# Kernel tuning notes

Measured on AMD Instinct MI355X. Metric: run time of the kernel, lower is better.

## Reference

```python
import jax, jax.numpy as jnp
import numpy as np

D_MODEL = 1024
NUM_HEADS = 16
D_K = D_MODEL // NUM_HEADS
B, S = 4, 2048


def setup_inputs() -> dict:
    key = jax.random.key(0)
    ks = jax.random.split(key, 11)
    scale = 1.0 / np.sqrt(D_MODEL)
    inp = {
        'query': jax.random.normal(ks[0], (B, S, D_MODEL), dtype=jnp.float32),
        'key':   jax.random.normal(ks[1], (B, S, D_MODEL), dtype=jnp.float32),
        'value': jax.random.normal(ks[2], (B, S, D_MODEL), dtype=jnp.float32),
        'Wq': jax.random.normal(ks[3], (D_MODEL, D_MODEL), dtype=jnp.float32) * scale,
        'bq': jnp.zeros((D_MODEL,), dtype=jnp.float32),
        'Wk': jax.random.normal(ks[4], (D_MODEL, D_MODEL), dtype=jnp.float32) * scale,
        'bk': jnp.zeros((D_MODEL,), dtype=jnp.float32),
        'Wv': jax.random.normal(ks[5], (D_MODEL, D_MODEL), dtype=jnp.float32) * scale,
        'bv': jnp.zeros((D_MODEL,), dtype=jnp.float32),
        'Wo': jax.random.normal(ks[6], (D_MODEL, D_MODEL), dtype=jnp.float32) * scale,
        'bo': jnp.zeros((D_MODEL,), dtype=jnp.float32),
    }
    return inp


def reference(query, key, value, Wq, bq, Wk, bk, Wv, bv, Wo, bo):
    b, sq, _ = query.shape
    sk = key.shape[1]
    # projections (torch Linear: x @ W.T + b; here W stored as [in, out])
    Q = query @ Wq + bq
    K = key @ Wk + bk
    V = value @ Wv + bv
    # split heads: [b, h, s, d_k]
    Q = Q.reshape(b, sq, NUM_HEADS, D_K).transpose(0, 2, 1, 3)
    K = K.reshape(b, sk, NUM_HEADS, D_K).transpose(0, 2, 1, 3)
    V = V.reshape(b, sk, NUM_HEADS, D_K).transpose(0, 2, 1, 3)
    # scaled dot-product attention (full [b,h,sq,sk] scores, as in source)
    scores = jnp.einsum('bhqd,bhkd->bhqk', Q, K) / jnp.sqrt(jnp.float32(D_K))
    attn = jax.nn.softmax(scores, axis=-1)
    out = jnp.einsum('bhqk,bhkd->bhqd', attn, V)
    out = out.transpose(0, 2, 1, 3).reshape(b, sq, D_MODEL)
    return out @ Wo + bo
```

## Files before the change

### kernel.cpp

```cpp
#include <hip/hip_runtime.h>
#include <hip/hip_bf16.h>
#include <stdint.h>

typedef __bf16 bf16x8 __attribute__((ext_vector_type(8)));
typedef __bf16 bf16x4 __attribute__((ext_vector_type(4)));
typedef float  f32x4  __attribute__((ext_vector_type(4)));
typedef unsigned short u16;

#define D_MODEL 1024
#define NUM_HEADS 16
#define DK 64
#define BATCH 4
#define SEQ 2048
#define M_TOTAL (BATCH*SEQ)
#define QK_SCALE 0.18033688011112042f

static __device__ __forceinline__ u16 f2bf(float f) {
    __bf16 h = (__bf16)f;
    return __builtin_bit_cast(u16, h);
}

#define ASYNC16(gptr, lptr) __builtin_amdgcn_global_load_lds( \
    (const __attribute__((address_space(1))) unsigned*)(uintptr_t)(gptr), \
    (__attribute__((address_space(3))) unsigned*)(unsigned)(uintptr_t)(lptr), 16, 0, 0)

__global__ void detect_dtype(const u16* __restrict__ q, unsigned* __restrict__ flag) {
    __shared__ int sh[256];
    int cnt = 0;
    for (int i = threadIdx.x; i < 8192; i += 256) {
        u16 v = q[2 * i];
        int e = (v >> 7) & 0xFF;
        if (e >= 100 && e <= 134) cnt++;
    }
    sh[threadIdx.x] = cnt;
    __syncthreads();
    for (int s = 128; s > 0; s >>= 1) {
        if (threadIdx.x < s) sh[threadIdx.x] += sh[threadIdx.x + s];
        __syncthreads();
    }
    if (threadIdx.x == 0) *flag = (sh[0] > 4096) ? 1u : 0u;
}

__global__ void transpose_w(const u16* __restrict__ W0, const u16* __restrict__ W1,
                            const u16* __restrict__ W2, const u16* __restrict__ W3,
                            u16* __restrict__ WT, const unsigned* __restrict__ flagp) {
    __shared__ u16 tile[32][33];
    const u16* W = (blockIdx.z == 0) ? W0 : (blockIdx.z == 1) ? W1 : (blockIdx.z == 2) ? W2 : W3;
    u16* T = WT + (size_t)blockIdx.z * D_MODEL * D_MODEL;
    bool is_bf16 = (*flagp != 0);
    int x = threadIdx.x, y0 = threadIdx.y;
    int bx = blockIdx.x * 32, by = blockIdx.y * 32;
    if (is_bf16) {
#pragma unroll
        for (int i = 0; i < 4; i++) {
            int y = y0 + i * 8;
            tile[y][x] = W[(size_t)(by + y) * D_MODEL + bx + x];
        }
    } else {
        const float* Wf = (const float*)W;
#pragma unroll
        for (int i = 0; i < 4; i++) {
            int y = y0 + i * 8;
            tile[y][x] = f2bf(Wf[(size_t)(by + y) * D_MODEL + bx + x]);
        }
    }
    __syncthreads();
#pragma unroll
    for (int i = 0; i < 4; i++) {
        int y = y0 + i * 8;
        T[(size_t)(bx + y) * D_MODEL + by + x] = tile[x][y];
    }
}

__global__ __launch_bounds__(256) void gemm_qkv(
    const u16* __restrict__ qin, const u16* __restrict__ kin, const u16* __restrict__ vin,
    const u16* __restrict__ WT,
    const u16* __restrict__ bq, const u16* __restrict__ bk, const u16* __restrict__ bv,
    u16* __restrict__ Qp, u16* __restrict__ Kp, u16* __restrict__ VpT,
    const unsigned* __restrict__ flagp)
{
    __shared__ __align__(16) u16 As[128 * 32];
    __shared__ __align__(16) u16 Bs[128 * 32];
    const int id  = blockIdx.x;
    const int xcd = id & 7, j = id >> 3;
    const int zy  = xcd * 24 + (j >> 3);
    const int bx  = j & 7;
    const int z   = zy >> 6, by = zy & 63;

    const u16* A    = (z == 0) ? qin : (z == 1) ? kin : vin;
    const u16* W    = WT + (size_t)z * 1048576;
    const u16* bias = (z == 0) ? bq : (z == 1) ? bk : bv;
    u16* C          = (z == 0) ? Qp : (z == 1) ? Kp : VpT;
    const int transV = (z == 2);
    const float oscale = (z == 0) ? QK_SCALE : 1.0f;

    const int tid  = threadIdx.x;
    const int lane = tid & 63, w = tid >> 6;
    const int quad = lane >> 4, l15 = lane & 15;
    const int wm = w >> 1, wn = w & 1;
    const int m_blk = by * 128, n_blk = bx * 128;
    const bool is_bf16 = (*flagp != 0);

    f32x4 acc[4][4] = {};

    const int ch0 = w * 2, ch1 = w * 2 + 1;
    const int sr0 = ch0 * 16 + (lane >> 2), sr1 = ch1 * 16 + (lane >> 2);
    const int skp = (lane & 3) * 8;
    const int frow = tid >> 1, fkp = (tid & 1) * 16;
    const float* Af = (const float*)A;

    for (int k0 = 0; k0 < D_MODEL; k0 += 32) {
        if (!is_bf16) {
            const float* src = Af + (size_t)(m_blk + frow) * D_MODEL + k0 + fkp;
            float4 f0 = ((const float4*)src)[0];
            float4 f1 = ((const float4*)src)[1];
            float4 f2 = ((const float4*)src)[2];
            float4 f3 = ((const float4*)src)[3];
            bf16x8 p0, p1;
            p0[0] = (__bf16)f0.x; p0[1] = (__bf16)f0.y; p0[2] = (__bf16)f0.z; p0[3] = (__bf16)f0.w;
            p0[4] = (__bf16)f1.x; p0[5] = (__bf16)f1.y; p0[6] = (__bf16)f1.z; p0[7] = (__bf16)f1.w;
            p1[0] = (__bf16)f2.x; p1[1] = (__bf16)f2.y; p1[2] = (__bf16)f2.z; p1[3] = (__bf16)f2.w;
            p1[4] = (__bf16)f3.x; p1[5] = (__bf16)f3.y; p1[6] = (__bf16)f3.z; p1[7] = (__bf16)f3.w;
            *(bf16x8*)&As[frow * 32 + fkp]     = p0;
            *(bf16x8*)&As[frow * 32 + fkp + 8] = p1;
        } else {
            ASYNC16(A + (size_t)(m_blk + sr0) * D_MODEL + k0 + skp, &As[ch0 * 512]);
            ASYNC16(A + (size_t)(m_blk + sr1) * D_MODEL + k0 + skp, &As[ch1 * 512]);
        }
        ASYNC16(W + (size_t)(n_blk + sr0) * D_MODEL + k0 + skp, &Bs[ch0 * 512]);
        ASYNC16(W + (size_t)(n_blk + sr1) * D_MODEL + k0 + skp, &Bs[ch1 * 512]);
        __syncthreads();

        bf16x8 af[4], bg[4];
#pragma unroll
        for (int sm = 0; sm < 4; sm++)
            af[sm] = *(const bf16x8*)&As[(wm * 64 + sm * 16 + l15) * 32 + quad * 8];
#pragma unroll
        for (int sn = 0; sn < 4; sn++)
            bg[sn] = *(const bf16x8*)&Bs[(wn * 64 + sn * 16 + l15) * 32 + quad * 8];
#pragma unroll
        for (int sm = 0; sm < 4; sm++)
#pragma unroll
            for (int sn = 0; sn < 4; sn++)
                acc[sm][sn] = __builtin_amdgcn_mfma_f32_16x16x32_bf16(af[sm], bg[sn], acc[sm][sn], 0, 0, 0);
        __syncthreads();
    }

#pragma unroll
    for (int sn = 0; sn < 4; sn++) {
        int n = n_blk + wn * 64 + sn * 16 + l15;
        float bvf = is_bf16 ? (float)((const __bf16*)bias)[n] : ((const float*)bias)[n];
#pragma unroll
        for (int sm = 0; sm < 4; sm++) {
            int mrow = m_blk + wm * 64 + sm * 16 + quad * 4;
            if (transV) {
                int b = mrow >> 11, s = mrow & 2047;
                ushort4 pk;
                pk.x = f2bf(acc[sm][sn][0] + bvf);
                pk.y = f2bf(acc[sm][sn][1] + bvf);
                pk.z = f2bf(acc[sm][sn][2] + bvf);
                pk.w = f2bf(acc[sm][sn][3] + bvf);
                *(ushort4*)(C + (size_t)b * D_MODEL * SEQ + (size_t)n * SEQ + s) = pk;
            } else {
#pragma unroll
                for (int r = 0; r < 4; r++)
                    C[(size_t)(mrow + r) * D_MODEL + n] = f2bf((acc[sm][sn][r] + bvf) * oscale);
            }
        }
    }
}

__global__ __launch_bounds__(256) void gemm_o(
    const u16* __restrict__ A, const u16* __restrict__ WT,
    const u16* __restrict__ bias, u16* __restrict__ C,
    const unsigned* __restrict__ flagp)
{
    __shared__ __align__(16) u16 As[64 * 32];
    __shared__ __align__(16) u16 Bs[128 * 32];
    const int id  = blockIdx.x;
    const int xcd = id & 7, j = id >> 3;
    const int by  = xcd * 16 + (j >> 3);
    const int bx  = j & 7;

    const int tid  = threadIdx.x;
    const int lane = tid & 63, w = tid >> 6;
    const int quad = lane >> 4, l15 = lane & 15;
    const int wm = w >> 1, wn = w & 1;
    const int m_blk = by * 64, n_blk = bx * 128;
    const bool is_bf16 = (*flagp != 0);

    f32x4 acc[2][4] = {};
    const int srow = lane >> 2, skp = (lane & 3) * 8;

    for (int k0 = 0; k0 < D_MODEL; k0 += 32) {
#pragma unroll
        for (int i = 0; i < 3; i++) {
            int c = w * 3 + i;
            if (c < 4)
                ASYNC16(A  + (size_t)(m_blk + c * 16 + srow) * D_MODEL + k0 + skp, &As[c * 512]);
            else
                ASYNC16(WT + (size_t)(n_blk + (c - 4) * 16 + srow) * D_MODEL + k0 + skp, &Bs[(c - 4) * 512]);
        }
        __syncthreads();

        bf16x8 af[2], bg[4];
#pragma unroll
        for (int sm = 0; sm < 2; sm++)
            af[sm] = *(const bf16x8*)&As[(wm * 32 + sm * 16 + l15) * 32 + quad * 8];
#pragma unroll
        for (int sn = 0; sn < 4; sn++)
            bg[sn] = *(const bf16x8*)&Bs[(wn * 64 + sn * 16 + l15) * 32 + quad * 8];
#pragma unroll
        for (int sm = 0; sm < 2; sm++)
#pragma unroll
            for (int sn = 0; sn < 4; sn++)
                acc[sm][sn] = __builtin_amdgcn_mfma_f32_16x16x32_bf16(af[sm], bg[sn], acc[sm][sn], 0, 0, 0);
        __syncthreads();
    }

#pragma unroll
    for (int sn = 0; sn < 4; sn++) {
        int n = n_blk + wn * 64 + sn * 16 + l15;
        float bvf = is_bf16 ? (float)((const __bf16*)bias)[n] : ((const float*)bias)[n];
#pragma unroll
        for (int sm = 0; sm < 2; sm++) {
            int mrow = m_blk + wm * 32 + sm * 16 + quad * 4;
            if (!is_bf16) {
                float* Cf = (float*)C;
#pragma unroll
                for (int r = 0; r < 4; r++)
                    Cf[(size_t)(mrow + r) * D_MODEL + n] = acc[sm][sn][r] + bvf;
            } else {
#pragma unroll
                for (int r = 0; r < 4; r++)
                    C[(size_t)(mrow + r) * D_MODEL + n] = f2bf(acc[sm][sn][r] + bvf);
            }
        }
    }
}

__global__ __launch_bounds__(256) void attn_kernel(
    const u16* __restrict__ Qp, const u16* __restrict__ Kp,
    const u16* __restrict__ VpT, u16* __restrict__ AO)
{
    __shared__ __align__(16) u16 Ks[2][64 * 64];
    __shared__ __align__(16) u16 Vs[2][64 * 64];
    __shared__ __align__(16) u16 Ps[4][32][68];
    const int id  = blockIdx.x;
    const int xcd = id & 7, j = id >> 3;
    const int bh  = xcd * 8 + (j >> 4);
    const int qx  = j & 15;

    const int tid  = threadIdx.x;
    const int lane = tid & 63, w = tid >> 6;
    const int quad = lane >> 4, l15 = lane & 15;
    const int b = bh >> 4, h = bh & 15;
    const int q_base = qx * 128 + w * 32;

    bf16x8 bQ[2][2];
#pragma unroll
    for (int sn = 0; sn < 2; sn++)
#pragma unroll
        for (int ds = 0; ds < 2; ds++)
            bQ[sn][ds] = *(const bf16x8*)(Qp + (size_t)(b * SEQ + q_base + sn * 16 + l15) * D_MODEL
                                              + h * DK + ds * 32 + quad * 8);

    float lsum[2] = {0.0f, 0.0f};
    f32x4 OT[2][4] = {};

    const u16* Kbase = Kp  + (size_t)(b * SEQ) * D_MODEL + h * DK;
    const u16* Vbase = VpT + (size_t)b * D_MODEL * SEQ + (size_t)(h * DK) * SEQ;

    const int c0   = w * 2;
    const int lrow = lane >> 3;
    const int ug   = (lane & 7) ^ lrow;
    const int swz  = l15 & 7;

    auto issue_tile = [&](int key0, int bf) {
#pragma unroll
        for (int i = 0; i < 2; i++) {
            int c = c0 + i;
            ASYNC16(Kbase + (size_t)(key0 + c * 8 + lrow) * D_MODEL + ug * 8, &Ks[bf][c * 512]);
            ASYNC16(Vbase + (size_t)(c * 8 + lrow) * SEQ + key0 + ug * 8,     &Vs[bf][c * 512]);
        }
    };

    issue_tile(0, 0);
    __syncthreads();

    for (int t = 0; t < SEQ / 64; t++) {
        const int cur = t & 1;
        if (t + 1 < SEQ / 64) issue_tile((t + 1) * 64, cur ^ 1);

#pragma unroll
        for (int kc = 0; kc < 4; kc++) {
            const int krow = (kc * 16 + l15) * 64;
            bf16x8 k0 = *(const bf16x8*)&Ks[cur][krow + ((quad ^ swz) * 8)];
            bf16x8 k1 = *(const bf16x8*)&Ks[cur][krow + (((4 + quad) ^ swz) * 8)];
#pragma unroll
            for (int sn = 0; sn < 2; sn++) {
                f32x4 s = {};
                s = __builtin_amdgcn_mfma_f32_16x16x32_bf16(k0, bQ[sn][0], s, 0, 0, 0);
                s = __builtin_amdgcn_mfma_f32_16x16x32_bf16(k1, bQ[sn][1], s, 0, 0, 0);
                float p0 = __builtin_amdgcn_exp2f(s[0]);
                float p1 = __builtin_amdgcn_exp2f(s[1]);
                float p2 = __builtin_amdgcn_exp2f(s[2]);
                float p3 = __builtin_amdgcn_exp2f(s[3]);
                lsum[sn] += (p0 + p1) + (p2 + p3);
                bf16x4 pk;
                pk[0] = (__bf16)p0; pk[1] = (__bf16)p1; pk[2] = (__bf16)p2; pk[3] = (__bf16)p3;
                *(bf16x4*)&Ps[w][sn * 16 + l15][kc * 16 + quad * 4] = pk;
            }
        }

#pragma unroll
        for (int kc2 = 0; kc2 < 2; kc2++) {
            bf16x8 bP0 = *(const bf16x8*)&Ps[w][l15][kc2 * 32 + quad * 8];
            bf16x8 bP1 = *(const bf16x8*)&Ps[w][16 + l15][kc2 * 32 + quad * 8];
#pragma unroll
            for (int nd = 0; nd < 4; nd++) {
                bf16x8 aV = *(const bf16x8*)&Vs[cur][(nd * 16 + l15) * 64
                                                    + (((kc2 * 4 + quad) ^ swz) * 8)];
                OT[0][nd] = __builtin_amdgcn_mfma_f32_16x16x32_bf16(aV, bP0, OT[0][nd], 0, 0, 0);
                OT[1][nd] = __builtin_amdgcn_mfma_f32_16x16x32_bf16(aV, bP1, OT[1][nd], 0, 0, 0);
            }
        }
        __syncthreads();
    }

#pragma unroll
    for (int sn = 0; sn < 2; sn++) {
        lsum[sn] += __shfl_xor(lsum[sn], 16, 64);
        lsum[sn] += __shfl_xor(lsum[sn], 32, 64);
        float rl = 1.0f / lsum[sn];
        size_t rowbase = (size_t)(b * SEQ + q_base + sn * 16 + l15) * D_MODEL + h * DK;
#pragma unroll
        for (int nd = 0; nd < 4; nd++) {
            ushort4 pk;
            pk.x = f2bf(OT[sn][nd][0] * rl);
            pk.y = f2bf(OT[sn][nd][1] * rl);
            pk.z = f2bf(OT[sn][nd][2] * rl);
            pk.w = f2bf(OT[sn][nd][3] * rl);
            *(ushort4*)(AO + rowbase + nd * 16 + quad * 4) = pk;
        }
    }
}

extern "C" void kernel_launch(void* const* d_in, const int* in_sizes, int n_in,
                              void* d_out, int out_size, void* d_ws, size_t ws_size,
                              hipStream_t stream) {
    const u16* q  = (const u16*)d_in[0];
    const u16* k  = (const u16*)d_in[1];
    const u16* v  = (const u16*)d_in[2];
    const u16* Wq = (const u16*)d_in[3];
    const u16* bq = (const u16*)d_in[4];
    const u16* Wk = (const u16*)d_in[5];
    const u16* bk = (const u16*)d_in[6];
    const u16* Wv = (const u16*)d_in[7];
    const u16* bv = (const u16*)d_in[8];
    const u16* Wo = (const u16*)d_in[9];
    const u16* bo = (const u16*)d_in[10];

    u16* ws   = (u16*)d_ws;
    unsigned* flagp = (unsigned*)ws;
    u16* WT   = ws + 16;
    u16* Qp   = WT + (size_t)4 * 1024 * 1024;
    u16* Kp   = Qp + (size_t)M_TOTAL * D_MODEL;
    u16* VpT  = Kp + (size_t)M_TOTAL * D_MODEL;
    u16* AO   = VpT + (size_t)M_TOTAL * D_MODEL;

    detect_dtype<<<1, 256, 0, stream>>>(q, flagp);
    transpose_w<<<dim3(32, 32, 4), dim3(32, 8), 0, stream>>>(Wq, Wk, Wv, Wo, WT, flagp);
    gemm_qkv<<<1536, 256, 0, stream>>>(q, k, v, WT, bq, bk, bv, Qp, Kp, VpT, flagp);
    attn_kernel<<<1024, 256, 0, stream>>>(Qp, Kp, VpT, AO);
    gemm_o<<<1024, 256, 0, stream>>>(AO, WT + 3 * 1048576, bo, (u16*)d_out, flagp);
}
```

Baseline: 417.2 us.

## Double-buffer LDS tiles in QKV and output projection GEMMs

```diff
diff --git a/kernel.cpp b/kernel.cpp
--- a/kernel.cpp
+++ b/kernel.cpp
@@ -23,6 +23,10 @@
 #define ASYNC16(gptr, lptr) __builtin_amdgcn_global_load_lds( \
     (const __attribute__((address_space(1))) unsigned*)(uintptr_t)(gptr), \
     (__attribute__((address_space(3))) unsigned*)(unsigned)(uintptr_t)(lptr), 16, 0, 0)
+
+#define PIPE_BARRIER() do { \
+    asm volatile("s_waitcnt vmcnt(0)" ::: "memory"); \
+    asm volatile("s_barrier" ::: "memory"); } while (0)
 
 __global__ void detect_dtype(const u16* __restrict__ q, unsigned* __restrict__ flag) {
     __shared__ int sh[256];
@@ -79,8 +83,8 @@
     u16* __restrict__ Qp, u16* __restrict__ Kp, u16* __restrict__ VpT,
     const unsigned* __restrict__ flagp)
 {
-    __shared__ __align__(16) u16 As[128 * 32];
-    __shared__ __align__(16) u16 Bs[128 * 32];
+    __shared__ __align__(16) u16 As[2][128 * 32];
+    __shared__ __align__(16) u16 Bs[2][128 * 32];
     const int id  = blockIdx.x;
     const int xcd = id & 7, j = id >> 3;
     const int zy  = xcd * 24 + (j >> 3);
@@ -106,11 +110,40 @@
     const int ch0 = w * 2, ch1 = w * 2 + 1;
     const int sr0 = ch0 * 16 + (lane >> 2), sr1 = ch1 * 16 + (lane >> 2);
     const int skp = (lane & 3) * 8;
-    const int frow = tid >> 1, fkp = (tid & 1) * 16;
-    const float* Af = (const float*)A;
-
-    for (int k0 = 0; k0 < D_MODEL; k0 += 32) {
-        if (!is_bf16) {
+
+    if (is_bf16) {
+        ASYNC16(A + (size_t)(m_blk + sr0) * D_MODEL + skp, &As[0][ch0 * 512]);
+        ASYNC16(A + (size_t)(m_blk + sr1) * D_MODEL + skp, &As[0][ch1 * 512]);
+        ASYNC16(W + (size_t)(n_blk + sr0) * D_MODEL + skp, &Bs[0][ch0 * 512]);
+        ASYNC16(W + (size_t)(n_blk + sr1) * D_MODEL + skp, &Bs[0][ch1 * 512]);
+
+        for (int t = 0; t < 32; ++t) {
+            const int cur = t & 1;
+            PIPE_BARRIER();
+            if (t + 1 < 32) {
+                const int k0 = (t + 1) * 32;
+                ASYNC16(A + (size_t)(m_blk + sr0) * D_MODEL + k0 + skp, &As[cur ^ 1][ch0 * 512]);
+                ASYNC16(A + (size_t)(m_blk + sr1) * D_MODEL + k0 + skp, &As[cur ^ 1][ch1 * 512]);
+                ASYNC16(W + (size_t)(n_blk + sr0) * D_MODEL + k0 + skp, &Bs[cur ^ 1][ch0 * 512]);
+                ASYNC16(W + (size_t)(n_blk + sr1) * D_MODEL + k0 + skp, &Bs[cur ^ 1][ch1 * 512]);
+            }
+            bf16x8 af[4], bg[4];
+#pragma unroll
+            for (int sm = 0; sm < 4; sm++)
+                af[sm] = *(const bf16x8*)&As[cur][(wm * 64 + sm * 16 + l15) * 32 + quad * 8];
+#pragma unroll
+            for (int sn = 0; sn < 4; sn++)
+                bg[sn] = *(const bf16x8*)&Bs[cur][(wn * 64 + sn * 16 + l15) * 32 + quad * 8];
+#pragma unroll
+            for (int sm = 0; sm < 4; sm++)
+#pragma unroll
+                for (int sn = 0; sn < 4; sn++)
+                    acc[sm][sn] = __builtin_amdgcn_mfma_f32_16x16x32_bf16(af[sm], bg[sn], acc[sm][sn], 0, 0, 0);
+        }
+    } else {
+        const int frow = tid >> 1, fkp = (tid & 1) * 16;
+        const float* Af = (const float*)A;
+        for (int k0 = 0; k0 < D_MODEL; k0 += 32) {
             const float* src = Af + (size_t)(m_blk + frow) * D_MODEL + k0 + fkp;
             float4 f0 = ((const float4*)src)[0];
             float4 f1 = ((const float4*)src)[1];
@@ -121,29 +154,25 @@
             p0[4] = (__bf16)f1.x; p0[5] = (__bf16)f1.y; p0[6] = (__bf16)f1.z; p0[7] = (__bf16)f1.w;
             p1[0] = (__bf16)f2.x; p1[1] = (__bf16)f2.y; p1[2] = (__bf16)f2.z; p1[3] = (__bf16)f2.w;
             p1[4] = (__bf16)f3.x; p1[5] = (__bf16)f3.y; p1[6] = (__bf16)f3.z; p1[7] = (__bf16)f3.w;
-            *(bf16x8*)&As[frow * 32 + fkp]     = p0;
-            *(bf16x8*)&As[frow * 32 + fkp + 8] = p1;
-        } else {
-            ASYNC16(A + (size_t)(m_blk + sr0) * D_MODEL + k0 + skp, &As[ch0 * 512]);
-            ASYNC16(A + (size_t)(m_blk + sr1) * D_MODEL + k0 + skp, &As[ch1 * 512]);
-        }
-        ASYNC16(W + (size_t)(n_blk + sr0) * D_MODEL + k0 + skp, &Bs[ch0 * 512]);
-        ASYNC16(W + (size_t)(n_blk + sr1) * D_MODEL + k0 + skp, &Bs[ch1 * 512]);
-        __syncthreads();
-
-        bf16x8 af[4], bg[4];
-#pragma unroll
-        for (int sm = 0; sm < 4; sm++)
-            af[sm] = *(const bf16x8*)&As[(wm * 64 + sm * 16 + l15) * 32 + quad * 8];
-#pragma unroll
-        for (int sn = 0; sn < 4; sn++)
-            bg[sn] = *(const bf16x8*)&Bs[(wn * 64 + sn * 16 + l15) * 32 + quad * 8];
-#pragma unroll
-        for (int sm = 0; sm < 4; sm++)
+            *(bf16x8*)&As[0][frow * 32 + fkp]     = p0;
+            *(bf16x8*)&As[0][frow * 32 + fkp + 8] = p1;
+            ASYNC16(W + (size_t)(n_blk + sr0) * D_MODEL + k0 + skp, &Bs[0][ch0 * 512]);
+            ASYNC16(W + (size_t)(n_blk + sr1) * D_MODEL + k0 + skp, &Bs[0][ch1 * 512]);
+            __syncthreads();
+            bf16x8 af[4], bg[4];
+#pragma unroll
+            for (int sm = 0; sm < 4; sm++)
+                af[sm] = *(const bf16x8*)&As[0][(wm * 64 + sm * 16 + l15) * 32 + quad * 8];
 #pragma unroll
             for (int sn = 0; sn < 4; sn++)
-                acc[sm][sn] = __builtin_amdgcn_mfma_f32_16x16x32_bf16(af[sm], bg[sn], acc[sm][sn], 0, 0, 0);
-        __syncthreads();
+                bg[sn] = *(const bf16x8*)&Bs[0][(wn * 64 + sn * 16 + l15) * 32 + quad * 8];
+#pragma unroll
+            for (int sm = 0; sm < 4; sm++)
+#pragma unroll
+                for (int sn = 0; sn < 4; sn++)
+                    acc[sm][sn] = __builtin_amdgcn_mfma_f32_16x16x32_bf16(af[sm], bg[sn], acc[sm][sn], 0, 0, 0);
+            __syncthreads();
+        }
     }
 
 #pragma unroll
@@ -175,8 +204,8 @@
     const u16* __restrict__ bias, u16* __restrict__ C,
     const unsigned* __restrict__ flagp)
 {
-    __shared__ __align__(16) u16 As[64 * 32];
-    __shared__ __align__(16) u16 Bs[128 * 32];
+    __shared__ __align__(16) u16 As[2][64 * 32];
+    __shared__ __align__(16) u16 Bs[2][128 * 32];
     const int id  = blockIdx.x;
     const int xcd = id & 7, j = id >> 3;
     const int by  = xcd * 16 + (j >> 3);
@@ -192,30 +221,35 @@
     f32x4 acc[2][4] = {};
     const int srow = lane >> 2, skp = (lane & 3) * 8;
 
-    for (int k0 = 0; k0 < D_MODEL; k0 += 32) {
+    auto issue = [&](int k0, int bf) {
 #pragma unroll
         for (int i = 0; i < 3; i++) {
             int c = w * 3 + i;
             if (c < 4)
-                ASYNC16(A  + (size_t)(m_blk + c * 16 + srow) * D_MODEL + k0 + skp, &As[c * 512]);
+                ASYNC16(A  + (size_t)(m_blk + c * 16 + srow) * D_MODEL + k0 + skp, &As[bf][c * 512]);
             else
-                ASYNC16(WT + (size_t)(n_blk + (c - 4) * 16 + srow) * D_MODEL + k0 + skp, &Bs[(c - 4) * 512]);
-        }
-        __syncthreads();
+                ASYNC16(WT + (size_t)(n_blk + (c - 4) * 16 + srow) * D_MODEL + k0 + skp, &Bs[bf][(c - 4) * 512]);
+        }
+    };
+
+    issue(0, 0);
+    for (int t = 0; t < 32; ++t) {
+        const int cur = t & 1;
+        PIPE_BARRIER();
+        if (t + 1 < 32) issue((t + 1) * 32, cur ^ 1);
 
         bf16x8 af[2], bg[4];
 #pragma unroll
         for (int sm = 0; sm < 2; sm++)
-            af[sm] = *(const bf16x8*)&As[(wm * 32 + sm * 16 + l15) * 32 + quad * 8];
+            af[sm] = *(const bf16x8*)&As[cur][(wm * 32 + sm * 16 + l15) * 32 + quad * 8];
 #pragma unroll
         for (int sn = 0; sn < 4; sn++)
-            bg[sn] = *(const bf16x8*)&Bs[(wn * 64 + sn * 16 + l15) * 32 + quad * 8];
+            bg[sn] = *(const bf16x8*)&Bs[cur][(wn * 64 + sn * 16 + l15) * 32 + quad * 8];
 #pragma unroll
         for (int sm = 0; sm < 2; sm++)
 #pragma unroll
             for (int sn = 0; sn < 4; sn++)
                 acc[sm][sn] = __builtin_amdgcn_mfma_f32_16x16x32_bf16(af[sm], bg[sn], acc[sm][sn], 0, 0, 0);
-        __syncthreads();
     }
 
 #pragma unroll
```

Result: slower. 432.1 us (+3.6%).

## Retile QKV and output GEMMs to 128x64x64 with XOR-swizzled LDS

Applied to the files above, without the earlier changes.

```diff
diff --git a/kernel.cpp b/kernel.cpp
--- a/kernel.cpp
+++ b/kernel.cpp
@@ -72,19 +72,19 @@
     }
 }
 
-__global__ __launch_bounds__(256) void gemm_qkv(
+__global__ __launch_bounds__(256, 4) void gemm_qkv(
     const u16* __restrict__ qin, const u16* __restrict__ kin, const u16* __restrict__ vin,
     const u16* __restrict__ WT,
     const u16* __restrict__ bq, const u16* __restrict__ bk, const u16* __restrict__ bv,
     u16* __restrict__ Qp, u16* __restrict__ Kp, u16* __restrict__ VpT,
     const unsigned* __restrict__ flagp)
 {
-    __shared__ __align__(16) u16 As[128 * 32];
-    __shared__ __align__(16) u16 Bs[128 * 32];
+    __shared__ __align__(16) u16 As[128 * 64];
+    __shared__ __align__(16) u16 Bs[64 * 64];
     const int id  = blockIdx.x;
     const int xcd = id & 7, j = id >> 3;
-    const int zy  = xcd * 24 + (j >> 3);
-    const int bx  = j & 7;
+    const int zy  = xcd * 24 + (j >> 4);
+    const int bx  = j & 15;
     const int z   = zy >> 6, by = zy & 63;
 
     const u16* A    = (z == 0) ? qin : (z == 1) ? kin : vin;
@@ -98,57 +98,75 @@
     const int lane = tid & 63, w = tid >> 6;
     const int quad = lane >> 4, l15 = lane & 15;
     const int wm = w >> 1, wn = w & 1;
-    const int m_blk = by * 128, n_blk = bx * 128;
+    const int m_blk = by * 128, n_blk = bx * 64;
     const bool is_bf16 = (*flagp != 0);
 
-    f32x4 acc[4][4] = {};
-
-    const int ch0 = w * 2, ch1 = w * 2 + 1;
-    const int sr0 = ch0 * 16 + (lane >> 2), sr1 = ch1 * 16 + (lane >> 2);
-    const int skp = (lane & 3) * 8;
-    const int frow = tid >> 1, fkp = (tid & 1) * 16;
-    const float* Af = (const float*)A;
-
-    for (int k0 = 0; k0 < D_MODEL; k0 += 32) {
-        if (!is_bf16) {
-            const float* src = Af + (size_t)(m_blk + frow) * D_MODEL + k0 + fkp;
-            float4 f0 = ((const float4*)src)[0];
-            float4 f1 = ((const float4*)src)[1];
-            float4 f2 = ((const float4*)src)[2];
-            float4 f3 = ((const float4*)src)[3];
-            bf16x8 p0, p1;
-            p0[0] = (__bf16)f0.x; p0[1] = (__bf16)f0.y; p0[2] = (__bf16)f0.z; p0[3] = (__bf16)f0.w;
-            p0[4] = (__bf16)f1.x; p0[5] = (__bf16)f1.y; p0[6] = (__bf16)f1.z; p0[7] = (__bf16)f1.w;
-            p1[0] = (__bf16)f2.x; p1[1] = (__bf16)f2.y; p1[2] = (__bf16)f2.z; p1[3] = (__bf16)f2.w;
-            p1[4] = (__bf16)f3.x; p1[5] = (__bf16)f3.y; p1[6] = (__bf16)f3.z; p1[7] = (__bf16)f3.w;
-            *(bf16x8*)&As[frow * 32 + fkp]     = p0;
-            *(bf16x8*)&As[frow * 32 + fkp + 8] = p1;
+    f32x4 acc[4][2] = {};
+
+    const int lrow = lane >> 3;
+    const int ug   = (lane & 7) ^ lrow;
+    const int r7   = l15 & 7;
+
+    for (int k0 = 0; k0 < D_MODEL; k0 += 64) {
+        if (is_bf16) {
+#pragma unroll
+            for (int i = 0; i < 4; i++) {
+                int c = w * 4 + i;
+                ASYNC16(A + (size_t)(m_blk + c * 8 + lrow) * D_MODEL + k0 + ug * 8,
+                        &As[c * 512]);
+            }
+#pragma unroll
+            for (int i = 0; i < 2; i++) {
+                int c = w * 2 + i;
+                ASYNC16(W + (size_t)(n_blk + c * 8 + lrow) * D_MODEL + k0 + ug * 8,
+                        &Bs[c * 512]);
+            }
         } else {
-            ASYNC16(A + (size_t)(m_blk + sr0) * D_MODEL + k0 + skp, &As[ch0 * 512]);
-            ASYNC16(A + (size_t)(m_blk + sr1) * D_MODEL + k0 + skp, &As[ch1 * 512]);
-        }
-        ASYNC16(W + (size_t)(n_blk + sr0) * D_MODEL + k0 + skp, &Bs[ch0 * 512]);
-        ASYNC16(W + (size_t)(n_blk + sr1) * D_MODEL + k0 + skp, &Bs[ch1 * 512]);
-        __syncthreads();
-
-        bf16x8 af[4], bg[4];
-#pragma unroll
-        for (int sm = 0; sm < 4; sm++)
-            af[sm] = *(const bf16x8*)&As[(wm * 64 + sm * 16 + l15) * 32 + quad * 8];
-#pragma unroll
-        for (int sn = 0; sn < 4; sn++)
-            bg[sn] = *(const bf16x8*)&Bs[(wn * 64 + sn * 16 + l15) * 32 + quad * 8];
-#pragma unroll
-        for (int sm = 0; sm < 4; sm++)
-#pragma unroll
-            for (int sn = 0; sn < 4; sn++)
-                acc[sm][sn] = __builtin_amdgcn_mfma_f32_16x16x32_bf16(af[sm], bg[sn], acc[sm][sn], 0, 0, 0);
-        __syncthreads();
-    }
-
-#pragma unroll
-    for (int sn = 0; sn < 4; sn++) {
-        int n = n_blk + wn * 64 + sn * 16 + l15;
+            const float* Af = (const float*)A;
+            int arow = tid >> 1, ub = (tid & 1) * 4;
+#pragma unroll
+            for (int u = 0; u < 4; u++) {
+                int uu = ub + u;
+                const float* src = Af + (size_t)(m_blk + arow) * D_MODEL + k0 + ((uu ^ (arow & 7)) * 8);
+                float4 f0 = ((const float4*)src)[0];
+                float4 f1 = ((const float4*)src)[1];
+                bf16x8 p;
+                p[0] = (__bf16)f0.x; p[1] = (__bf16)f0.y; p[2] = (__bf16)f0.z; p[3] = (__bf16)f0.w;
+                p[4] = (__bf16)f1.x; p[5] = (__bf16)f1.y; p[6] = (__bf16)f1.z; p[7] = (__bf16)f1.w;
+                *(bf16x8*)&As[arow * 64 + uu * 8] = p;
+            }
+#pragma unroll
+            for (int i = 0; i < 2; i++) {
+                int c = w * 2 + i;
+                ASYNC16(W + (size_t)(n_blk + c * 8 + lrow) * D_MODEL + k0 + ug * 8,
+                        &Bs[c * 512]);
+            }
+        }
+        __syncthreads();
+
+#pragma unroll
+        for (int ks = 0; ks < 2; ks++) {
+            bf16x8 af[4], bg[2];
+#pragma unroll
+            for (int sm = 0; sm < 4; sm++)
+                af[sm] = *(const bf16x8*)&As[(wm * 64 + sm * 16 + l15) * 64
+                                             + (((ks * 4 + quad) ^ r7) * 8)];
+#pragma unroll
+            for (int sn = 0; sn < 2; sn++)
+                bg[sn] = *(const bf16x8*)&Bs[(wn * 32 + sn * 16 + l15) * 64
+                                             + (((ks * 4 + quad) ^ r7) * 8)];
+#pragma unroll
+            for (int sm = 0; sm < 4; sm++)
+#pragma unroll
+                for (int sn = 0; sn < 2; sn++)
+                    acc[sm][sn] = __builtin_amdgcn_mfma_f32_16x16x32_bf16(af[sm], bg[sn], acc[sm][sn], 0, 0, 0);
+        }
+        __syncthreads();
+    }
+
+#pragma unroll
+    for (int sn = 0; sn < 2; sn++) {
+        int n = n_blk + wn * 32 + sn * 16 + l15;
         float bvf = is_bf16 ? (float)((const __bf16*)bias)[n] : ((const float*)bias)[n];
 #pragma unroll
         for (int sm = 0; sm < 4; sm++) {
@@ -170,61 +188,70 @@
     }
 }
 
-__global__ __launch_bounds__(256) void gemm_o(
+__global__ __launch_bounds__(256, 4) void gemm_o(
     const u16* __restrict__ A, const u16* __restrict__ WT,
     const u16* __restrict__ bias, u16* __restrict__ C,
     const unsigned* __restrict__ flagp)
 {
-    __shared__ __align__(16) u16 As[64 * 32];
-    __shared__ __align__(16) u16 Bs[128 * 32];
+    __shared__ __align__(16) u16 As[128 * 64];
+    __shared__ __align__(16) u16 Bs[64 * 64];
     const int id  = blockIdx.x;
     const int xcd = id & 7, j = id >> 3;
-    const int by  = xcd * 16 + (j >> 3);
-    const int bx  = j & 7;
+    const int by  = xcd * 8 + (j >> 4);
+    const int bx  = j & 15;
 
     const int tid  = threadIdx.x;
     const int lane = tid & 63, w = tid >> 6;
     const int quad = lane >> 4, l15 = lane & 15;
     const int wm = w >> 1, wn = w & 1;
-    const int m_blk = by * 64, n_blk = bx * 128;
+    const int m_blk = by * 128, n_blk = bx * 64;
     const bool is_bf16 = (*flagp != 0);
 
-    f32x4 acc[2][4] = {};
-    const int srow = lane >> 2, skp = (lane & 3) * 8;
-
-    for (int k0 = 0; k0 < D_MODEL; k0 += 32) {
-#pragma unroll
-        for (int i = 0; i < 3; i++) {
-            int c = w * 3 + i;
-            if (c < 4)
-                ASYNC16(A  + (size_t)(m_blk + c * 16 + srow) * D_MODEL + k0 + skp, &As[c * 512]);
-            else
-                ASYNC16(WT + (size_t)(n_blk + (c - 4) * 16 + srow) * D_MODEL + k0 + skp, &Bs[(c - 4) * 512]);
-        }
-        __syncthreads();
-
-        bf16x8 af[2], bg[4];
-#pragma unroll
-        for (int sm = 0; sm < 2; sm++)
-            af[sm] = *(const bf16x8*)&As[(wm * 32 + sm * 16 + l15) * 32 + quad * 8];
-#pragma unroll
-        for (int sn = 0; sn < 4; sn++)
-            bg[sn] = *(const bf16x8*)&Bs[(wn * 64 + sn * 16 + l15) * 32 + quad * 8];
-#pragma unroll
-        for (int sm = 0; sm < 2; sm++)
-#pragma unroll
-            for (int sn = 0; sn < 4; sn++)
-                acc[sm][sn] = __builtin_amdgcn_mfma_f32_16x16x32_bf16(af[sm], bg[sn], acc[sm][sn], 0, 0, 0);
-        __syncthreads();
-    }
-
-#pragma unroll
-    for (int sn = 0; sn < 4; sn++) {
-        int n = n_blk + wn * 64 + sn * 16 + l15;
+    f32x4 acc[4][2] = {};
+    const int lrow = lane >> 3;
+    const int ug   = (lane & 7) ^ lrow;
+    const int r7   = l15 & 7;
+
+    for (int k0 = 0; k0 < D_MODEL; k0 += 64) {
+#pragma unroll
+        for (int i = 0; i < 4; i++) {
+            int c = w * 4 + i;
+            ASYNC16(A + (size_t)(m_blk + c * 8 + lrow) * D_MODEL + k0 + ug * 8, &As[c * 512]);
+        }
+#pragma unroll
+        for (int i = 0; i < 2; i++) {
+            int c = w * 2 + i;
+            ASYNC16(WT + (size_t)(n_blk + c * 8 + lrow) * D_MODEL + k0 + ug * 8, &Bs[c * 512]);
+        }
+        __syncthreads();
+
+#pragma unroll
+        for (int ks = 0; ks < 2; ks++) {
+            bf16x8 af[4], bg[2];
+#pragma unroll
+            for (int sm = 0; sm < 4; sm++)
+                af[sm] = *(const bf16x8*)&As[(wm * 64 + sm * 16 + l15) * 64
+                                             + (((ks * 4 + quad) ^ r7) * 8)];
+#pragma unroll
+            for (int sn = 0; sn < 2; sn++)
+                bg[sn] = *(const bf16x8*)&Bs[(wn * 32 + sn * 16 + l15) * 64
+                                             + (((ks * 4 + quad) ^ r7) * 8)];
+#pragma unroll
+            for (int sm = 0; sm < 4; sm++)
+#pragma unroll
+                for (int sn = 0; sn < 2; sn++)
+                    acc[sm][sn] = __builtin_amdgcn_mfma_f32_16x16x32_bf16(af[sm], bg[sn], acc[sm][sn], 0, 0, 0);
+        }
+        __syncthreads();
+    }
+
+#pragma unroll
+    for (int sn = 0; sn < 2; sn++) {
+        int n = n_blk + wn * 32 + sn * 16 + l15;
         float bvf = is_bf16 ? (float)((const __bf16*)bias)[n] : ((const float*)bias)[n];
 #pragma unroll
-        for (int sm = 0; sm < 2; sm++) {
-            int mrow = m_blk + wm * 32 + sm * 16 + quad * 4;
+        for (int sm = 0; sm < 4; sm++) {
+            int mrow = m_blk + wm * 64 + sm * 16 + quad * 4;
             if (!is_bf16) {
                 float* Cf = (float*)C;
 #pragma unroll
@@ -371,7 +398,7 @@
 
     detect_dtype<<<1, 256, 0, stream>>>(q, flagp);
     transpose_w<<<dim3(32, 32, 4), dim3(32, 8), 0, stream>>>(Wq, Wk, Wv, Wo, WT, flagp);
-    gemm_qkv<<<1536, 256, 0, stream>>>(q, k, v, WT, bq, bk, bv, Qp, Kp, VpT, flagp);
+    gemm_qkv<<<3072, 256, 0, stream>>>(q, k, v, WT, bq, bk, bv, Qp, Kp, VpT, flagp);
     attn_kernel<<<1024, 256, 0, stream>>>(Qp, Kp, VpT, AO);
     gemm_o<<<1024, 256, 0, stream>>>(AO, WT + 3 * 1048576, bo, (u16*)d_out, flagp);
 }
```

Result: slower. 507.3 us (+21.6%).
